# Kernel tuning notes

Measured on AMD Instinct MI355X. Metric: run time of the kernel, lower is better.

The kernel has to match this reference:

```python
import jax, jax.numpy as jnp
import numpy as np

D_MODEL = 1024
N_HEADS = 16
D_K = D_MODEL // N_HEADS


def setup_inputs() -> dict:
    key = jax.random.key(0)
    ks = jax.random.split(key, 9)
    B, S = 4, 2048
    scale = 1.0 / np.sqrt(D_MODEL)
    x = jax.random.normal(ks[0], (B, S, D_MODEL), dtype=jnp.float32)
    # Linear params: weight [out,in] (torch convention), bias [out]
    wq = jax.random.uniform(ks[1], (D_MODEL, D_MODEL), jnp.float32, -scale, scale)
    bq = jax.random.uniform(ks[2], (D_MODEL,), jnp.float32, -scale, scale)
    wk = jax.random.uniform(ks[3], (D_MODEL, D_MODEL), jnp.float32, -scale, scale)
    bk = jax.random.uniform(ks[4], (D_MODEL,), jnp.float32, -scale, scale)
    wv = jax.random.uniform(ks[5], (D_MODEL, D_MODEL), jnp.float32, -scale, scale)
    bv = jax.random.uniform(ks[6], (D_MODEL,), jnp.float32, -scale, scale)
    wo = jax.random.uniform(ks[7], (D_MODEL, D_MODEL), jnp.float32, -scale, scale)
    bo = jax.random.uniform(ks[8], (D_MODEL,), jnp.float32, -scale, scale)
    return {"x": x, "wq": wq, "bq": bq, "wk": wk, "bk": bk,
            "wv": wv, "bv": bv, "wo": wo, "bo": bo}


def reference(x, wq, bq, wk, bk, wv, bv, wo, bo):
    B, S, _ = x.shape
    # QKV projections (torch Linear: x @ W^T + b)
    q = x @ wq.T + bq
    k = x @ wk.T + bk
    v = x @ wv.T + bv
    # [B, H, S, D_K]
    q = q.reshape(B, S, N_HEADS, D_K).transpose(0, 2, 1, 3)
    k = k.reshape(B, S, N_HEADS, D_K).transpose(0, 2, 1, 3)
    v = v.reshape(B, S, N_HEADS, D_K).transpose(0, 2, 1, 3)
    scores = jnp.einsum('bhqd,bhkd->bhqk', q, k) / jnp.sqrt(jnp.float32(D_K))
    attn = jax.nn.softmax(scores, axis=-1)
    out = jnp.einsum('bhqk,bhkd->bhqd', attn, v)
    out = out.transpose(0, 2, 1, 3).reshape(B, S, D_MODEL)
    return out @ wo.T + bo
```

## Files before the change

### kernel.cpp

```cpp
#include <hip/hip_runtime.h>

#define DMODEL 1024
#define NHEADS 16
#define DK 64
#define BATCH 4
#define SEQ 2048
#define MROWS (BATCH * SEQ)
#define NT 16

typedef __attribute__((ext_vector_type(8))) short bf16x8;
typedef __attribute__((ext_vector_type(8))) unsigned short u16x8;
typedef __attribute__((ext_vector_type(4))) unsigned short u16x4;
typedef __attribute__((ext_vector_type(4))) float f32x4;
typedef __attribute__((ext_vector_type(16))) float f32x16;
typedef __attribute__((ext_vector_type(2))) unsigned int u32x2;
typedef __attribute__((ext_vector_type(4))) unsigned int u32x4;

using gld_gptr = const __attribute__((address_space(1))) unsigned int*;
using gld_lptr = __attribute__((address_space(3))) unsigned int*;

#define QSCALE 0.18033688011112042f

__device__ inline unsigned short f32_bf16(float f) {
    unsigned int u = __float_as_uint(f);
    u += 0x7FFFu + ((u >> 16) & 1u);
    return (unsigned short)(u >> 16);
}

__device__ inline unsigned int cvtpk_bf16(float a, float b) {
    unsigned int r;
    asm("v_cvt_pk_bf16_f32 %0, %1, %2" : "=v"(r) : "v"(a), "v"(b));
    return r;
}

__device__ inline f32x16 fz16() {
    f32x16 v;
#pragma unroll
    for (int i = 0; i < 16; ++i) v[i] = 0.f;
    return v;
}

struct Conv5 {
    const float* s[5];
    unsigned short* d[5];
};

__global__ __launch_bounds__(256) void conv5_kernel(Conv5 c) {
    int bx = blockIdx.x;
    int which, idx;
    if (bx < 4096) { which = 0; idx = bx; }
    else { which = 1 + ((bx - 4096) >> 9); idx = (bx - 4096) & 511; }
    int i = idx * 256 + threadIdx.x;
    const float4* s = (const float4*)(c.s[which] + (size_t)i * 8);
    float4 a = s[0], b = s[1];
    u16x8 o;
    o[0] = f32_bf16(a.x); o[1] = f32_bf16(a.y); o[2] = f32_bf16(a.z); o[3] = f32_bf16(a.w);
    o[4] = f32_bf16(b.x); o[5] = f32_bf16(b.y); o[6] = f32_bf16(b.z); o[7] = f32_bf16(b.w);
    *(u16x8*)(c.d[which] + (size_t)i * 8) = o;
}


__device__ __forceinline__ void stage_half(const unsigned short* mat, int row0, int step,
                                           char* lds_half, int tid) {
#pragma unroll
    for (int rnd = 0; rnd < 2; ++rnd) {
        int rl = rnd * 64 + (tid >> 3);
        int c16 = (tid & 7) ^ (rl & 7);
        const unsigned short* g = mat + (size_t)(row0 + rl) * DMODEL + step * 64 + c16 * 8;
        __builtin_amdgcn_global_load_lds((gld_gptr)g,
            (gld_lptr)(lds_half + rnd * 8192 + (tid >> 6) * 1024), 16, 0, 0);
    }
}

__device__ __forceinline__ bf16x8 lds_frag(const char* base, int row, int kk, int l) {
    int kb = kk * 64 + (l >> 4) * 16;
    return *(const bf16x8*)(base + row * 128 + (kb ^ ((row & 7) << 4)));
}

template <int QP>
__device__ __forceinline__ void phase_reads(const char* Ab, const char* Bb,
                                            bf16x8 (&breg)[4][2], bf16x8 (&areg)[2],
                                            int wm, int wn, int l) {
    int l15 = l & 15;
    if constexpr (QP == 0) {
#pragma unroll
        for (int nt = 0; nt < 4; ++nt)
#pragma unroll
            for (int kk = 0; kk < 2; ++kk)
                breg[nt][kk] = lds_frag(Bb, wn * 64 + nt * 16 + l15, kk, l);
    }
#pragma unroll
    for (int kk = 0; kk < 2; ++kk)
        areg[kk] = lds_frag(Ab, wm * 64 + QP * 16 + l15, kk, l);
}

template <int QP>
__device__ __forceinline__ void phase_mfma(bf16x8 (&areg)[2], bf16x8 (&breg)[4][2],
                                           f32x4 (&acc)[4][4]) {
    __builtin_amdgcn_s_setprio(1);
#pragma unroll
    for (int nt = 0; nt < 4; ++nt) {
        acc[QP][nt] = __builtin_amdgcn_mfma_f32_16x16x32_bf16(
            areg[0], breg[nt][0], acc[QP][nt], 0, 0, 0);
        acc[QP][nt] = __builtin_amdgcn_mfma_f32_16x16x32_bf16(
            areg[1], breg[nt][1], acc[QP][nt], 0, 0, 0);
    }
    __builtin_amdgcn_s_setprio(0);
}

#define GBAR() __builtin_amdgcn_s_barrier()
#define VMC2() asm volatile("s_waitcnt vmcnt(2)" ::: "memory")

template <bool F32OUT>
__device__ __forceinline__ void gemm_core(const unsigned short* __restrict__ Am,
                                          const unsigned short* __restrict__ Bm,
                                          const float* __restrict__ bias, void* Cv,
                                          float scl, int m0, int n0) {
    __shared__ __align__(16) char lds[98304];
    char* A0 = lds;
    char* B0 = lds + 32768;
    char* A1 = lds + 49152;
    char* B1 = lds + 81920;

    int tid = threadIdx.x, l = tid & 63, w = tid >> 6;
    int wm = w >> 1, wn = w & 1;

    f32x4 acc[4][4];
#pragma unroll
    for (int i = 0; i < 4; ++i)
#pragma unroll
        for (int j = 0; j < 4; ++j) acc[i][j] = (f32x4){0.f, 0.f, 0.f, 0.f};

    stage_half(Am, m0,       0, A0,         tid);
    stage_half(Am, m0 + 128, 0, A0 + 16384, tid);
    stage_half(Bm, n0,       0, B0,         tid);
    stage_half(Bm, n0,       1, B1,         tid);
    VMC2();
    GBAR();

    bf16x8 breg[4][2];
    for (int i = 0; i < NT / 2; ++i) {
        int E = 2 * i;
        bf16x8 areg[2];
        phase_reads<0>(A0, B0, breg, areg, wm, wn, l);
        stage_half(Am, m0,       (E + 1) & 15, A1, tid);
        GBAR(); phase_mfma<0>(areg, breg, acc); GBAR();

        phase_reads<1>(A0, B0, breg, areg, wm, wn, l);
        stage_half(Am, m0 + 128, (E + 1) & 15, A1 + 16384, tid);
        GBAR(); phase_mfma<1>(areg, breg, acc); GBAR();

        phase_reads<2>(A0, B0, breg, areg, wm, wn, l);
        stage_half(Bm, n0,       (E + 2) & 15, B0, tid);
        GBAR(); phase_mfma<2>(areg, breg, acc); GBAR();

        phase_reads<3>(A0, B0, breg, areg, wm, wn, l);
        GBAR(); phase_mfma<3>(areg, breg, acc);
        VMC2();
        GBAR();

        phase_reads<0>(A1, B1, breg, areg, wm, wn, l);
        stage_half(Am, m0,       (E + 2) & 15, A0, tid);
        GBAR(); phase_mfma<0>(areg, breg, acc); GBAR();

        phase_reads<1>(A1, B1, breg, areg, wm, wn, l);
        stage_half(Am, m0 + 128, (E + 2) & 15, A0 + 16384, tid);
        GBAR(); phase_mfma<1>(areg, breg, acc); GBAR();

        phase_reads<2>(A1, B1, breg, areg, wm, wn, l);
        stage_half(Bm, n0,       (E + 3) & 15, B1, tid);
        GBAR(); phase_mfma<2>(areg, breg, acc); GBAR();

        phase_reads<3>(A1, B1, breg, areg, wm, wn, l);
        GBAR(); phase_mfma<3>(areg, breg, acc);
        VMC2();
        GBAR();
    }

    int lm = l >> 4, ln = l & 15;
#pragma unroll
    for (int nt = 0; nt < 4; ++nt) {
        int col = n0 + wn * 64 + nt * 16 + ln;
        float bv = bias[col];
#pragma unroll
        for (int mt = 0; mt < 4; ++mt)
#pragma unroll
            for (int r = 0; r < 4; ++r) {
                int row = m0 + wm * 64 + mt * 16 + lm * 4 + r;
                float v = (acc[mt][nt][r] + bv) * scl;
                if constexpr (F32OUT)
                    ((float*)Cv)[(size_t)row * DMODEL + col] = v;
                else
                    ((unsigned short*)Cv)[(size_t)row * DMODEL + col] = f32_bf16(v);
            }
    }
}

struct QkvPtrs {
    const unsigned short* w[3];
    const float* b[3];
    unsigned short* c[3];
    float scale[3];
};

__global__ __launch_bounds__(512, 2) void gemm_qkv8(const unsigned short* __restrict__ A, QkvPtrs p) {
    int sel = blockIdx.y >> 3;
    int n0 = (blockIdx.y & 7) * 128;
    int m0 = blockIdx.x * 256;
    gemm_core<false>(A, p.w[sel], p.b[sel], p.c[sel], p.scale[sel], m0, n0);
}

__global__ __launch_bounds__(512, 2) void gemm_out8(const unsigned short* __restrict__ A,
                                                    const unsigned short* __restrict__ B,
                                                    const float* __restrict__ bias,
                                                    float* __restrict__ C) {
    gemm_core<true>(A, B, bias, C, 1.0f, blockIdx.x * 256, blockIdx.y * 128);
}

#define BUILD_PW(dst, pv, o)                                                        \
    {                                                                               \
        unsigned int wa_ = cvtpk_bf16(pv[(o) + 0], pv[(o) + 1]);                    \
        unsigned int wb_ = cvtpk_bf16(pv[(o) + 2], pv[(o) + 3]);                    \
        unsigned int wc_ = cvtpk_bf16(pv[(o) + 4], pv[(o) + 5]);                    \
        unsigned int wd_ = cvtpk_bf16(pv[(o) + 6], pv[(o) + 7]);                    \
        u32x2 ra_ = __builtin_amdgcn_permlane32_swap(wa_, wc_, false, false);       \
        u32x2 rb_ = __builtin_amdgcn_permlane32_swap(wb_, wd_, false, false);       \
        dst = (u32x4){ra_[0], rb_[0], ra_[1], rb_[1]};                              \
    }

#define ABAR() asm volatile("s_barrier" ::: "memory")
#define AVMC0() asm volatile("s_waitcnt vmcnt(0)" ::: "memory")

__device__ __forceinline__ void stage_k(const unsigned short* kp, int kt,
                                        unsigned short* kbuf, int l, int w) {
#pragma unroll
    for (int i = 0; i < 2; ++i) {
        int chunk = w + i * 4;
        int srccol = (l & 7) ^ (l >> 3);
        const unsigned short* g = kp + (size_t)(kt * 64 + chunk * 8 + (l >> 3)) * DMODEL + srccol * 8;
        __builtin_amdgcn_global_load_lds((gld_gptr)g, (gld_lptr)(kbuf + chunk * 512), 16, 0, 0);
    }
}

__device__ __forceinline__ void load_v(const unsigned short* vp, int kt, int tid,
                                       bf16x8& va, bf16x8& vb) {
    int kvp = (tid & 31) * 2;
    int d0 = (tid >> 5) * 8;
    va = *(const bf16x8*)&vp[(size_t)(kt * 64 + kvp) * DMODEL + d0];
    vb = *(const bf16x8*)&vp[(size_t)(kt * 64 + kvp + 1) * DMODEL + d0];
}

__device__ __forceinline__ void write_v(unsigned short* vbuf, int tid, bf16x8 va, bf16x8 vb) {
    int kvp = (tid & 31) * 2;
    int d0 = (tid >> 5) * 8;
#pragma unroll
    for (int j = 0; j < 8; ++j) {
        int d = d0 + j;
        unsigned int val = ((unsigned int)(unsigned short)va[j]) |
                           (((unsigned int)(unsigned short)vb[j]) << 16);
        int byt = d * 128 + (((kvp >> 3) ^ (d & 7)) << 4) + (kvp & 7) * 2;
        *(unsigned int*)((char*)vbuf + byt) = val;
    }
}

__global__ __launch_bounds__(256, 2) void attn_kernel(const unsigned short* __restrict__ Q,
                                                      const unsigned short* __restrict__ Km,
                                                      const unsigned short* __restrict__ Vm,
                                                      unsigned short* __restrict__ O) {
    __shared__ unsigned short Klds[2][64 * 64];
    __shared__ unsigned short Vt[2][64 * 64];

    int flat = blockIdx.y * gridDim.x + blockIdx.x;
    int xcd = flat & 7, idx = flat >> 3;
    int bh = xcd * 8 + (idx & 7);
    int qt = idx >> 3;
    int b = bh >> 4, h = bh & 15;
    int tid = threadIdx.x, l = tid & 63, w = tid >> 6;
    int lq = l & 31, hf = l >> 5;
    const size_t base = ((size_t)b * SEQ) * DMODEL + (size_t)h * DK;
    const unsigned short* qp = Q + base;
    const unsigned short* kp = Km + base;
    const unsigned short* vp = Vm + base;
    int q0 = qt * 256 + w * 64;

    bf16x8 qf[2][4];
#pragma unroll
    for (int sb = 0; sb < 2; ++sb)
#pragma unroll
        for (int ks = 0; ks < 4; ++ks)
            qf[sb][ks] = *(const bf16x8*)&qp[(size_t)(q0 + sb * 32 + lq) * DMODEL + ks * 16 + hf * 8];

    f32x16 accO[2][2];
    accO[0][0] = fz16(); accO[0][1] = fz16(); accO[1][0] = fz16(); accO[1][1] = fz16();
    float l_r[2] = {0.f, 0.f};

    bf16x8 va, vb;
    stage_k(kp, 0, Klds[0], l, w);
    load_v(vp, 0, tid, va, vb);
    AVMC0();
    write_v(Vt[0], tid, va, vb);
    ABAR();

    for (int kt = 0; kt < SEQ / 64; ++kt) {
        int cur = kt & 1, nxt = cur ^ 1;
        bool pre = (kt + 1 < SEQ / 64);
        if (pre) {
            stage_k(kp, kt + 1, Klds[nxt], l, w);
            load_v(vp, kt + 1, tid, va, vb);
        }

        f32x16 s[2][2];
        s[0][0] = fz16(); s[0][1] = fz16(); s[1][0] = fz16(); s[1][1] = fz16();
        __builtin_amdgcn_s_setprio(1);
#pragma unroll
        for (int ks = 0; ks < 4; ++ks) {
            int col16 = ks * 2 + hf;
            bf16x8 kf0 = *(const bf16x8*)((const char*)Klds[cur] + lq * 128 + ((col16 ^ (lq & 7)) << 4));
            bf16x8 kf1 = *(const bf16x8*)((const char*)Klds[cur] + (lq + 32) * 128 + ((col16 ^ (lq & 7)) << 4));
            s[0][0] = __builtin_amdgcn_mfma_f32_32x32x16_bf16(kf0, qf[0][ks], s[0][0], 0, 0, 0);
            s[0][1] = __builtin_amdgcn_mfma_f32_32x32x16_bf16(kf1, qf[0][ks], s[0][1], 0, 0, 0);
            s[1][0] = __builtin_amdgcn_mfma_f32_32x32x16_bf16(kf0, qf[1][ks], s[1][0], 0, 0, 0);
            s[1][1] = __builtin_amdgcn_mfma_f32_32x32x16_bf16(kf1, qf[1][ks], s[1][1], 0, 0, 0);
        }
        __builtin_amdgcn_s_setprio(0);

        u32x4 pw[2][4];
#pragma unroll
        for (int sb = 0; sb < 2; ++sb) {
            float rs = 0.f;
#pragma unroll
            for (int r = 0; r < 16; ++r) { s[sb][0][r] = __builtin_amdgcn_exp2f(s[sb][0][r]); rs += s[sb][0][r]; }
#pragma unroll
            for (int r = 0; r < 16; ++r) { s[sb][1][r] = __builtin_amdgcn_exp2f(s[sb][1][r]); rs += s[sb][1][r]; }
            rs += __shfl_xor(rs, 32);
            l_r[sb] += rs;
            BUILD_PW(pw[sb][0], s[sb][0], 0);
            BUILD_PW(pw[sb][1], s[sb][0], 8);
            BUILD_PW(pw[sb][2], s[sb][1], 0);
            BUILD_PW(pw[sb][3], s[sb][1], 8);
        }

        __builtin_amdgcn_s_setprio(1);
#pragma unroll
        for (int ks = 0; ks < 4; ++ks) {
            int col16 = ks * 2 + hf;
            int d1 = 32 + lq;
            bf16x8 vf0 = *(const bf16x8*)((const char*)Vt[cur] + lq * 128 + ((col16 ^ (lq & 7)) << 4));
            bf16x8 vf1 = *(const bf16x8*)((const char*)Vt[cur] + d1 * 128 + ((col16 ^ (d1 & 7)) << 4));
            bf16x8 pf0 = *(bf16x8*)&pw[0][ks];
            bf16x8 pf1 = *(bf16x8*)&pw[1][ks];
            accO[0][0] = __builtin_amdgcn_mfma_f32_32x32x16_bf16(vf0, pf0, accO[0][0], 0, 0, 0);
            accO[0][1] = __builtin_amdgcn_mfma_f32_32x32x16_bf16(vf1, pf0, accO[0][1], 0, 0, 0);
            accO[1][0] = __builtin_amdgcn_mfma_f32_32x32x16_bf16(vf0, pf1, accO[1][0], 0, 0, 0);
            accO[1][1] = __builtin_amdgcn_mfma_f32_32x32x16_bf16(vf1, pf1, accO[1][1], 0, 0, 0);
        }
        __builtin_amdgcn_s_setprio(0);

        if (pre) {
            AVMC0();
            write_v(Vt[nxt], tid, va, vb);
        }
        ABAR();
    }

#pragma unroll
    for (int sb = 0; sb < 2; ++sb) {
        float inv = 1.0f / l_r[sb];
        unsigned short* op = O + base + (size_t)(q0 + sb * 32 + lq) * DMODEL;
#pragma unroll
        for (int db = 0; db < 2; ++db)
#pragma unroll
            for (int rg = 0; rg < 4; ++rg) {
                int dbase = db * 32 + rg * 8 + hf * 4;
                u16x4 ov;
#pragma unroll
                for (int j = 0; j < 4; ++j) ov[j] = f32_bf16(accO[sb][db][rg * 4 + j] * inv);
                *(u16x4*)&op[dbase] = ov;
            }
    }
}

extern "C" void kernel_launch(void* const* d_in, const int* in_sizes, int n_in,
                              void* d_out, int out_size, void* d_ws, size_t ws_size,
                              hipStream_t stream) {
    (void)in_sizes; (void)n_in; (void)out_size; (void)ws_size;
    const float* x  = (const float*)d_in[0];
    const float* wq = (const float*)d_in[1];
    const float* bq = (const float*)d_in[2];
    const float* wk = (const float*)d_in[3];
    const float* bk = (const float*)d_in[4];
    const float* wv = (const float*)d_in[5];
    const float* bv = (const float*)d_in[6];
    const float* wo = (const float*)d_in[7];
    const float* bo = (const float*)d_in[8];
    float* out = (float*)d_out;
    char* ws = (char*)d_ws;

    unsigned short* xb  = (unsigned short*)(ws);
    unsigned short* wqb = (unsigned short*)(ws + (16ull << 20));
    unsigned short* wkb = (unsigned short*)(ws + (18ull << 20));
    unsigned short* wvb = (unsigned short*)(ws + (20ull << 20));
    unsigned short* wob = (unsigned short*)(ws + (22ull << 20));
    unsigned short* qb  = (unsigned short*)(ws + (24ull << 20));
    unsigned short* kb  = (unsigned short*)(ws + (40ull << 20));
    unsigned short* vb  = (unsigned short*)(ws + (56ull << 20));
    unsigned short* ob  = xb;

    Conv5 cv;
    cv.s[0] = x;  cv.d[0] = xb;
    cv.s[1] = wq; cv.d[1] = wqb;
    cv.s[2] = wk; cv.d[2] = wkb;
    cv.s[3] = wv; cv.d[3] = wvb;
    cv.s[4] = wo; cv.d[4] = wob;
    conv5_kernel<<<4096 + 4 * 512, 256, 0, stream>>>(cv);

    QkvPtrs p;
    p.w[0] = wqb; p.w[1] = wkb; p.w[2] = wvb;
    p.b[0] = bq;  p.b[1] = bk;  p.b[2] = bv;
    p.c[0] = qb;  p.c[1] = kb;  p.c[2] = vb;
    p.scale[0] = QSCALE; p.scale[1] = 1.0f; p.scale[2] = 1.0f;
    gemm_qkv8<<<dim3(32, 24), 512, 0, stream>>>(xb, p);

    attn_kernel<<<dim3(8, 64), 256, 0, stream>>>(qb, kb, vb, ob);

    gemm_out8<<<dim3(32, 8), 512, 0, stream>>>(ob, wob, bo, out);
}
```

Measured before the change: 183.1 us.

## Software-pipeline attention loop: overlap PV of previous tile with exp of current

Restructures the attention main loop so the P·V MFMAs for the previous KV tile are interleaved with the exp2/pack softmax work of the current tile. A prologue computes the first tile's probabilities and an epilogue finishes the last PV. K and V LDS buffers go from double to triple buffering so the previous V tile stays resident. The s_setprio hints are dropped. This costs more LDS (48KB per block) and extra registers, which may reduce occupancy at the 2-blocks-per-CU bound.

```diff
diff --git a/kernel.cpp b/kernel.cpp
--- a/kernel.cpp
+++ b/kernel.cpp
@@ -59,7 +59,6 @@
     *(u16x8*)(c.d[which] + (size_t)i * 8) = o;
 }
 
-
 __device__ __forceinline__ void stage_half(const unsigned short* mat, int row0, int step,
                                            char* lds_half, int tid) {
 #pragma unroll
@@ -267,8 +266,8 @@
                                                       const unsigned short* __restrict__ Km,
                                                       const unsigned short* __restrict__ Vm,
                                                       unsigned short* __restrict__ O) {
-    __shared__ unsigned short Klds[2][64 * 64];
-    __shared__ unsigned short Vt[2][64 * 64];
+    __shared__ unsigned short Klds[3][64 * 64];
+    __shared__ unsigned short Vt[3][64 * 64];
 
     int flat = blockIdx.y * gridDim.x + blockIdx.x;
     int xcd = flat & 7, idx = flat >> 3;
@@ -293,74 +292,132 @@
     f32x16 accO[2][2];
     accO[0][0] = fz16(); accO[0][1] = fz16(); accO[1][0] = fz16(); accO[1][1] = fz16();
     float l_r[2] = {0.f, 0.f};
+    u32x4 pwp[2][4];
 
     bf16x8 va, vb;
+    f32x16 s[2][2];
+
     stage_k(kp, 0, Klds[0], l, w);
     load_v(vp, 0, tid, va, vb);
     AVMC0();
     write_v(Vt[0], tid, va, vb);
     ABAR();
 
-    for (int kt = 0; kt < SEQ / 64; ++kt) {
-        int cur = kt & 1, nxt = cur ^ 1;
+    stage_k(kp, 1, Klds[1], l, w);
+    load_v(vp, 1, tid, va, vb);
+    s[0][0] = fz16(); s[0][1] = fz16(); s[1][0] = fz16(); s[1][1] = fz16();
+#pragma unroll
+    for (int ks = 0; ks < 4; ++ks) {
+        int col16 = ks * 2 + hf;
+        bf16x8 kf0 = *(const bf16x8*)((const char*)Klds[0] + lq * 128 + ((col16 ^ (lq & 7)) << 4));
+        bf16x8 kf1 = *(const bf16x8*)((const char*)Klds[0] + (lq + 32) * 128 + ((col16 ^ (lq & 7)) << 4));
+        s[0][0] = __builtin_amdgcn_mfma_f32_32x32x16_bf16(kf0, qf[0][ks], s[0][0], 0, 0, 0);
+        s[0][1] = __builtin_amdgcn_mfma_f32_32x32x16_bf16(kf1, qf[0][ks], s[0][1], 0, 0, 0);
+        s[1][0] = __builtin_amdgcn_mfma_f32_32x32x16_bf16(kf0, qf[1][ks], s[1][0], 0, 0, 0);
+        s[1][1] = __builtin_amdgcn_mfma_f32_32x32x16_bf16(kf1, qf[1][ks], s[1][1], 0, 0, 0);
+    }
+#pragma unroll
+    for (int sb = 0; sb < 2; ++sb) {
+        float rs = 0.f;
+#pragma unroll
+        for (int r = 0; r < 16; ++r) { s[sb][0][r] = __builtin_amdgcn_exp2f(s[sb][0][r]); rs += s[sb][0][r]; }
+#pragma unroll
+        for (int r = 0; r < 16; ++r) { s[sb][1][r] = __builtin_amdgcn_exp2f(s[sb][1][r]); rs += s[sb][1][r]; }
+        rs += __shfl_xor(rs, 32);
+        l_r[sb] += rs;
+        BUILD_PW(pwp[sb][0], s[sb][0], 0);
+        BUILD_PW(pwp[sb][1], s[sb][0], 8);
+        BUILD_PW(pwp[sb][2], s[sb][1], 0);
+        BUILD_PW(pwp[sb][3], s[sb][1], 8);
+    }
+    AVMC0();
+    write_v(Vt[1], tid, va, vb);
+    ABAR();
+
+    for (int kt = 1; kt < SEQ / 64; ++kt) {
+        int bc = kt % 3;
+        int bp = (kt + 2) % 3;
+        int bn = (kt + 1) % 3;
         bool pre = (kt + 1 < SEQ / 64);
         if (pre) {
-            stage_k(kp, kt + 1, Klds[nxt], l, w);
+            stage_k(kp, kt + 1, &Klds[0][0] + bn * 4096, l, w);
             load_v(vp, kt + 1, tid, va, vb);
         }
 
-        f32x16 s[2][2];
         s[0][0] = fz16(); s[0][1] = fz16(); s[1][0] = fz16(); s[1][1] = fz16();
-        __builtin_amdgcn_s_setprio(1);
+        const char* Kb = (const char*)(&Klds[0][0] + bc * 4096);
 #pragma unroll
         for (int ks = 0; ks < 4; ++ks) {
             int col16 = ks * 2 + hf;
-            bf16x8 kf0 = *(const bf16x8*)((const char*)Klds[cur] + lq * 128 + ((col16 ^ (lq & 7)) << 4));
-            bf16x8 kf1 = *(const bf16x8*)((const char*)Klds[cur] + (lq + 32) * 128 + ((col16 ^ (lq & 7)) << 4));
+            bf16x8 kf0 = *(const bf16x8*)(Kb + lq * 128 + ((col16 ^ (lq & 7)) << 4));
+            bf16x8 kf1 = *(const bf16x8*)(Kb + (lq + 32) * 128 + ((col16 ^ (lq & 7)) << 4));
             s[0][0] = __builtin_amdgcn_mfma_f32_32x32x16_bf16(kf0, qf[0][ks], s[0][0], 0, 0, 0);
             s[0][1] = __builtin_amdgcn_mfma_f32_32x32x16_bf16(kf1, qf[0][ks], s[0][1], 0, 0, 0);
             s[1][0] = __builtin_amdgcn_mfma_f32_32x32x16_bf16(kf0, qf[1][ks], s[1][0], 0, 0, 0);
             s[1][1] = __builtin_amdgcn_mfma_f32_32x32x16_bf16(kf1, qf[1][ks], s[1][1], 0, 0, 0);
         }
-        __builtin_amdgcn_s_setprio(0);
-
-        u32x4 pw[2][4];
-#pragma unroll
-        for (int sb = 0; sb < 2; ++sb) {
-            float rs = 0.f;
-#pragma unroll
-            for (int r = 0; r < 16; ++r) { s[sb][0][r] = __builtin_amdgcn_exp2f(s[sb][0][r]); rs += s[sb][0][r]; }
-#pragma unroll
-            for (int r = 0; r < 16; ++r) { s[sb][1][r] = __builtin_amdgcn_exp2f(s[sb][1][r]); rs += s[sb][1][r]; }
-            rs += __shfl_xor(rs, 32);
-            l_r[sb] += rs;
-            BUILD_PW(pw[sb][0], s[sb][0], 0);
-            BUILD_PW(pw[sb][1], s[sb][0], 8);
-            BUILD_PW(pw[sb][2], s[sb][1], 0);
-            BUILD_PW(pw[sb][3], s[sb][1], 8);
-        }
-
-        __builtin_amdgcn_s_setprio(1);
+
+        const char* Vb = (const char*)(&Vt[0][0] + bp * 4096);
+        float rs0 = 0.f, rs1 = 0.f;
 #pragma unroll
         for (int ks = 0; ks < 4; ++ks) {
             int col16 = ks * 2 + hf;
             int d1 = 32 + lq;
-            bf16x8 vf0 = *(const bf16x8*)((const char*)Vt[cur] + lq * 128 + ((col16 ^ (lq & 7)) << 4));
-            bf16x8 vf1 = *(const bf16x8*)((const char*)Vt[cur] + d1 * 128 + ((col16 ^ (d1 & 7)) << 4));
-            bf16x8 pf0 = *(bf16x8*)&pw[0][ks];
-            bf16x8 pf1 = *(bf16x8*)&pw[1][ks];
+            bf16x8 vf0 = *(const bf16x8*)(Vb + lq * 128 + ((col16 ^ (lq & 7)) << 4));
+            bf16x8 vf1 = *(const bf16x8*)(Vb + d1 * 128 + ((col16 ^ (d1 & 7)) << 4));
+            bf16x8 pf0 = *(bf16x8*)&pwp[0][ks];
+            bf16x8 pf1 = *(bf16x8*)&pwp[1][ks];
+            accO[0][0] = __builtin_amdgcn_mfma_f32_32x32x16_bf16(vf0, pf0, accO[0][0], 0, 0, 0);
+            accO[0][1] = __builtin_amdgcn_mfma_f32_32x32x16_bf16(vf1, pf0, accO[0][1], 0, 0, 0);
+            accO[1][0] = __builtin_amdgcn_mfma_f32_32x32x16_bf16(vf0, pf1, accO[1][0], 0, 0, 0);
+            accO[1][1] = __builtin_amdgcn_mfma_f32_32x32x16_bf16(vf1, pf1, accO[1][1], 0, 0, 0);
+
+            const int blk = ks >> 1, off = (ks & 1) * 8;
+#pragma unroll
+            for (int r = 0; r < 8; ++r) {
+                float e = __builtin_amdgcn_exp2f(s[0][blk][off + r]);
+                s[0][blk][off + r] = e; rs0 += e;
+            }
+#pragma unroll
+            for (int r = 0; r < 8; ++r) {
+                float e = __builtin_amdgcn_exp2f(s[1][blk][off + r]);
+                s[1][blk][off + r] = e; rs1 += e;
+            }
+            u32x4 t0, t1;
+            BUILD_PW(t0, s[0][blk], off);
+            BUILD_PW(t1, s[1][blk], off);
+            pwp[0][ks] = t0;
+            pwp[1][ks] = t1;
+        }
+        rs0 += __shfl_xor(rs0, 32);
+        rs1 += __shfl_xor(rs1, 32);
+        l_r[0] += rs0;
+        l_r[1] += rs1;
+
+        if (pre) {
+            AVMC0();
+            write_v(&Vt[0][0] + bn * 4096, tid, va, vb);
+        }
+        ABAR();
+    }
+
+    {
+        int bp = (31) % 3 == 0 ? 0 : ((31 % 3 == 1) ? 1 : 2);
+        const char* Vb = (const char*)(&Vt[0][0] + (31 % 3) * 4096);
+        (void)bp;
+#pragma unroll
+        for (int ks = 0; ks < 4; ++ks) {
+            int col16 = ks * 2 + hf;
+            int d1 = 32 + lq;
+            bf16x8 vf0 = *(const bf16x8*)(Vb + lq * 128 + ((col16 ^ (lq & 7)) << 4));
+            bf16x8 vf1 = *(const bf16x8*)(Vb + d1 * 128 + ((col16 ^ (d1 & 7)) << 4));
+            bf16x8 pf0 = *(bf16x8*)&pwp[0][ks];
+            bf16x8 pf1 = *(bf16x8*)&pwp[1][ks];
             accO[0][0] = __builtin_amdgcn_mfma_f32_32x32x16_bf16(vf0, pf0, accO[0][0], 0, 0, 0);
             accO[0][1] = __builtin_amdgcn_mfma_f32_32x32x16_bf16(vf1, pf0, accO[0][1], 0, 0, 0);
             accO[1][0] = __builtin_amdgcn_mfma_f32_32x32x16_bf16(vf0, pf1, accO[1][0], 0, 0, 0);
             accO[1][1] = __builtin_amdgcn_mfma_f32_32x32x16_bf16(vf1, pf1, accO[1][1], 0, 0, 0);
         }
-        __builtin_amdgcn_s_setprio(0);
-
-        if (pre) {
-            AVMC0();
-            write_v(Vt[nxt], tid, va, vb);
-        }
-        ABAR();
     }
 
 #pragma unroll
```

Result: no change. 179.6 us (-1.9%).
